# Optimization experiments

Hardware: AMD Instinct MI355X
Metric: run time of the kernel (lower is better)

## Reference

```python
import jax, jax.numpy as jnp
import numpy as np

B, H, W, C = 128, 28, 28, 512


def setup_inputs() -> dict:
    key = jax.random.key(0)
    k1, k2 = jax.random.split(key)
    x = jax.random.normal(k1, (B, H, W, C), dtype=jnp.float32)
    t_p = jax.random.uniform(k2, (H, W, H, W), dtype=jnp.float32)
    return {"x": x, "t_p": t_p}


def reference(x, t_p):
    # x: [B,H,W,C] NHWC; t_p: [H,W,H,W] spatial template bank.
    Bx, Hx, Wx, Cx = x.shape
    # Global-spatial max_pool_with_argmax == argmax over flattened H*W per (b,c).
    flat = x.reshape(Bx, Hx * Wx, Cx)
    idx = jnp.argmax(flat, axis=1)            # [B,C] first-max, like TF
    h = idx // Wx                              # [B,C] row of spatial argmax
    w = idx % Wx                               # [B,C] col of spatial argmax
    # Per-(b,c) template gather: t_p[h,w] -> [B,C,H,W]
    templates = t_p[h, w]
    templates = jnp.transpose(templates, (0, 2, 3, 1))  # [B,H,W,C]
    masked = jax.nn.relu(x * templates)
    return masked, x, templates
```

## Files before the change

### kernel.cpp

```cpp
#include <hip/hip_runtime.h>

#define Bn 128
#define Hn 28
#define Wn 28
#define Cn 512
#define Pn (Hn * Wn)
#define NCH 8
#define CB (Bn / NCH)
#define SCH 28
#define PCH (Pn / SCH)
#define ARGB ((CB / 2) * SCH)
#define MSKB (CB * 14)
#define PPB 56
#define PPT 28

typedef float f4 __attribute__((ext_vector_type(4)));

__device__ __forceinline__ void nt_store4(float* p, float a, float b, float c, float d) {
    f4 v = {a, b, c, d};
    __builtin_nontemporal_store(v, reinterpret_cast<f4*>(p));
}
__device__ __forceinline__ f4 nt_load4(const float* p) {
    return __builtin_nontemporal_load(reinterpret_cast<const f4*>(p));
}

__global__ __launch_bounds__(256) void pipe(const float* __restrict__ x,
                                            const float* __restrict__ tp,
                                            float* __restrict__ o0,
                                            float* __restrict__ o1,
                                            float* __restrict__ o2,
                                            uint2* __restrict__ part,
                                            int k, int nArg) {
    __shared__ int sidx[Cn];

    if ((int)blockIdx.x < nArg) {
        int blk = blockIdx.x;
        int s  = blk % SCH;
        int bp = blk / SCH;
        int bl = bp * 2 + (threadIdx.x >> 7);
        int b  = k * CB + bl;
        int c0 = (threadIdx.x & 127) * 4;

        size_t base = (size_t)b * Pn * Cn + c0;
        int p0 = s * PCH;

        float b0 = -INFINITY, b1 = -INFINITY, b2 = -INFINITY, b3 = -INFINITY;
        int i0 = p0, i1 = p0, i2 = p0, i3 = p0;
#pragma unroll 7
        for (int i = 0; i < PCH; ++i) {
            float4 v = *reinterpret_cast<const float4*>(x + base + (size_t)(p0 + i) * Cn);
            if (v.x > b0) { b0 = v.x; i0 = p0 + i; }
            if (v.y > b1) { b1 = v.y; i1 = p0 + i; }
            if (v.z > b2) { b2 = v.z; i2 = p0 + i; }
            if (v.w > b3) { b3 = v.w; i3 = p0 + i; }
        }
        uint2* o = part + (((size_t)(k & 1) * SCH + s) * CB + bl) * Cn + c0;
        o[0] = make_uint2(__float_as_uint(b0), (unsigned)i0);
        o[1] = make_uint2(__float_as_uint(b1), (unsigned)i1);
        o[2] = make_uint2(__float_as_uint(b2), (unsigned)i2);
        o[3] = make_uint2(__float_as_uint(b3), (unsigned)i3);
        return;
    }

    int blk = blockIdx.x - nArg;
    int pc = blk % 14;
    int bl = blk / 14;
    int b  = (k - 1) * CB + bl;
    int t  = threadIdx.x;

    if (t < 128) {
        int c0 = t * 4;
        const uint2* pp = part + ((size_t)((k - 1) & 1) * SCH * CB + bl) * Cn + c0;
        float v0 = -INFINITY, v1 = -INFINITY, v2 = -INFINITY, v3 = -INFINITY;
        int j0 = 0, j1 = 0, j2 = 0, j3 = 0;
#pragma unroll
        for (int s = 0; s < SCH; ++s) {
            const uint2* q = pp + (size_t)s * (CB * Cn);
            uint4 a = *reinterpret_cast<const uint4*>(q);
            uint4 c = *reinterpret_cast<const uint4*>(q + 2);
            float f0 = __uint_as_float(a.x), f1 = __uint_as_float(a.z);
            float f2 = __uint_as_float(c.x), f3 = __uint_as_float(c.z);
            if (f0 > v0) { v0 = f0; j0 = (int)a.y; }
            if (f1 > v1) { v1 = f1; j1 = (int)a.w; }
            if (f2 > v2) { v2 = f2; j2 = (int)c.y; }
            if (f3 > v3) { v3 = f3; j3 = (int)c.w; }
        }
        sidx[c0 + 0] = j0;
        sidx[c0 + 1] = j1;
        sidx[c0 + 2] = j2;
        sidx[c0 + 3] = j3;
    }
    __syncthreads();

    int ci = t & 127;
    int c0 = ci * 4;
    int ph = t >> 7;
    int p0 = pc * PPB + ph * PPT;

    int4 iv = *reinterpret_cast<const int4*>(sidx + c0);
    const float* t0p = tp + (size_t)iv.x * Pn;
    const float* t1p = tp + (size_t)iv.y * Pn;
    const float* t2p = tp + (size_t)iv.z * Pn;
    const float* t3p = tp + (size_t)iv.w * Pn;

    size_t xbase = (size_t)b * Pn * Cn + c0;

#pragma unroll
    for (int j = 0; j < PPT; j += 4) {
        int p = p0 + j;
        float4 ta = *reinterpret_cast<const float4*>(t0p + p);
        float4 tb = *reinterpret_cast<const float4*>(t1p + p);
        float4 tc = *reinterpret_cast<const float4*>(t2p + p);
        float4 td = *reinterpret_cast<const float4*>(t3p + p);
        f4 x0 = nt_load4(x + xbase + (size_t)(p + 0) * Cn);
        f4 x1 = nt_load4(x + xbase + (size_t)(p + 1) * Cn);
        f4 x2 = nt_load4(x + xbase + (size_t)(p + 2) * Cn);
        f4 x3 = nt_load4(x + xbase + (size_t)(p + 3) * Cn);

        size_t q0 = xbase + (size_t)(p + 0) * Cn;
        size_t q1 = xbase + (size_t)(p + 1) * Cn;
        size_t q2 = xbase + (size_t)(p + 2) * Cn;
        size_t q3 = xbase + (size_t)(p + 3) * Cn;

        nt_store4(o1 + q0, x0.x, x0.y, x0.z, x0.w);
        nt_store4(o1 + q1, x1.x, x1.y, x1.z, x1.w);
        nt_store4(o1 + q2, x2.x, x2.y, x2.z, x2.w);
        nt_store4(o1 + q3, x3.x, x3.y, x3.z, x3.w);
        nt_store4(o0 + q0, fmaxf(x0.x * ta.x, 0.f), fmaxf(x0.y * tb.x, 0.f),
                           fmaxf(x0.z * tc.x, 0.f), fmaxf(x0.w * td.x, 0.f));
        nt_store4(o0 + q1, fmaxf(x1.x * ta.y, 0.f), fmaxf(x1.y * tb.y, 0.f),
                           fmaxf(x1.z * tc.y, 0.f), fmaxf(x1.w * td.y, 0.f));
        nt_store4(o0 + q2, fmaxf(x2.x * ta.z, 0.f), fmaxf(x2.y * tb.z, 0.f),
                           fmaxf(x2.z * tc.z, 0.f), fmaxf(x2.w * td.z, 0.f));
        nt_store4(o0 + q3, fmaxf(x3.x * ta.w, 0.f), fmaxf(x3.y * tb.w, 0.f),
                           fmaxf(x3.z * tc.w, 0.f), fmaxf(x3.w * td.w, 0.f));
        nt_store4(o2 + q0, ta.x, tb.x, tc.x, td.x);
        nt_store4(o2 + q1, ta.y, tb.y, tc.y, td.y);
        nt_store4(o2 + q2, ta.z, tb.z, tc.z, td.z);
        nt_store4(o2 + q3, ta.w, tb.w, tc.w, td.w);
    }
}

extern "C" void kernel_launch(void* const* d_in, const int* in_sizes, int n_in,
                              void* d_out, int out_size, void* d_ws, size_t ws_size,
                              hipStream_t stream) {
    const float* x  = (const float*)d_in[0];
    const float* tp = (const float*)d_in[1];

    const size_t N = (size_t)Bn * Pn * Cn;
    float* o0 = (float*)d_out;
    float* o1 = o0 + N;
    float* o2 = o0 + 2 * N;

    uint2* part = (uint2*)d_ws;

    for (int k = 0; k <= NCH; ++k) {
        int nArg  = (k < NCH) ? ARGB : 0;
        int nMask = (k > 0) ? MSKB : 0;
        pipe<<<nArg + nMask, 256, 0, stream>>>(x, tp, o0, o1, o2, part, k, nArg);
    }
}
```

Baseline: 195.7 us.

## Replace chunked pipelined launches with two separate argmax and mask kernels

Drops the 9-launch software pipeline that overlapped the argmax pass for one batch chunk with the mask/output pass for the previous chunk. It now runs one argmax-partial kernel over all batches with 8 spatial splits and 128-thread blocks, then a single mask kernel. This removes per-launch overhead and the mixed-role blocks. It gives up the cross-chunk overlap and the L2 reuse of x between the two passes, so x is likely read from HBM twice.

```diff
diff --git a/kernel.cpp b/kernel.cpp
--- a/kernel.cpp
+++ b/kernel.cpp
@@ -5,12 +5,8 @@
 #define Wn 28
 #define Cn 512
 #define Pn (Hn * Wn)
-#define NCH 8
-#define CB (Bn / NCH)
-#define SCH 28
+#define SCH 8
 #define PCH (Pn / SCH)
-#define ARGB ((CB / 2) * SCH)
-#define MSKB (CB * 14)
 #define PPB 56
 #define PPT 28
 
@@ -24,58 +20,52 @@
     return __builtin_nontemporal_load(reinterpret_cast<const f4*>(p));
 }
 
-__global__ __launch_bounds__(256) void pipe(const float* __restrict__ x,
-                                            const float* __restrict__ tp,
-                                            float* __restrict__ o0,
-                                            float* __restrict__ o1,
-                                            float* __restrict__ o2,
-                                            uint2* __restrict__ part,
-                                            int k, int nArg) {
+__global__ void argmax_partial(const float* __restrict__ x,
+                               uint2* __restrict__ part) {
+    int s = blockIdx.x & (SCH - 1);
+    int b = blockIdx.x >> 3;
+    int c0 = threadIdx.x * 4;
+
+    const float* xp = x + (size_t)b * Pn * Cn + c0;
+    int p0 = s * PCH;
+
+    float b0 = -INFINITY, b1 = -INFINITY, b2 = -INFINITY, b3 = -INFINITY;
+    int i0 = p0, i1 = p0, i2 = p0, i3 = p0;
+#pragma unroll 7
+    for (int i = 0; i < PCH; ++i) {
+        float4 v = *reinterpret_cast<const float4*>(xp + (size_t)(p0 + i) * Cn);
+        if (v.x > b0) { b0 = v.x; i0 = p0 + i; }
+        if (v.y > b1) { b1 = v.y; i1 = p0 + i; }
+        if (v.z > b2) { b2 = v.z; i2 = p0 + i; }
+        if (v.w > b3) { b3 = v.w; i3 = p0 + i; }
+    }
+    uint4* o = reinterpret_cast<uint4*>(part + ((size_t)s * Bn + b) * Cn + c0);
+    o[0] = make_uint4(__float_as_uint(b0), (unsigned)i0,
+                      __float_as_uint(b1), (unsigned)i1);
+    o[1] = make_uint4(__float_as_uint(b2), (unsigned)i2,
+                      __float_as_uint(b3), (unsigned)i3);
+}
+
+__global__ void mask_outputs(const float* __restrict__ x,
+                             const float* __restrict__ tp,
+                             const uint2* __restrict__ part,
+                             float* __restrict__ o0,
+                             float* __restrict__ o1,
+                             float* __restrict__ o2) {
     __shared__ int sidx[Cn];
 
-    if ((int)blockIdx.x < nArg) {
-        int blk = blockIdx.x;
-        int s  = blk % SCH;
-        int bp = blk / SCH;
-        int bl = bp * 2 + (threadIdx.x >> 7);
-        int b  = k * CB + bl;
-        int c0 = (threadIdx.x & 127) * 4;
-
-        size_t base = (size_t)b * Pn * Cn + c0;
-        int p0 = s * PCH;
-
-        float b0 = -INFINITY, b1 = -INFINITY, b2 = -INFINITY, b3 = -INFINITY;
-        int i0 = p0, i1 = p0, i2 = p0, i3 = p0;
-#pragma unroll 7
-        for (int i = 0; i < PCH; ++i) {
-            float4 v = *reinterpret_cast<const float4*>(x + base + (size_t)(p0 + i) * Cn);
-            if (v.x > b0) { b0 = v.x; i0 = p0 + i; }
-            if (v.y > b1) { b1 = v.y; i1 = p0 + i; }
-            if (v.z > b2) { b2 = v.z; i2 = p0 + i; }
-            if (v.w > b3) { b3 = v.w; i3 = p0 + i; }
-        }
-        uint2* o = part + (((size_t)(k & 1) * SCH + s) * CB + bl) * Cn + c0;
-        o[0] = make_uint2(__float_as_uint(b0), (unsigned)i0);
-        o[1] = make_uint2(__float_as_uint(b1), (unsigned)i1);
-        o[2] = make_uint2(__float_as_uint(b2), (unsigned)i2);
-        o[3] = make_uint2(__float_as_uint(b3), (unsigned)i3);
-        return;
-    }
-
-    int blk = blockIdx.x - nArg;
-    int pc = blk % 14;
-    int bl = blk / 14;
-    int b  = (k - 1) * CB + bl;
+    int pc = blockIdx.x % 14;
+    int b  = blockIdx.x / 14;
     int t  = threadIdx.x;
 
     if (t < 128) {
         int c0 = t * 4;
-        const uint2* pp = part + ((size_t)((k - 1) & 1) * SCH * CB + bl) * Cn + c0;
+        const uint2* pp = part + (size_t)b * Cn + c0;
         float v0 = -INFINITY, v1 = -INFINITY, v2 = -INFINITY, v3 = -INFINITY;
         int j0 = 0, j1 = 0, j2 = 0, j3 = 0;
 #pragma unroll
         for (int s = 0; s < SCH; ++s) {
-            const uint2* q = pp + (size_t)s * (CB * Cn);
+            const uint2* q = pp + (size_t)s * (Bn * Cn);
             uint4 a = *reinterpret_cast<const uint4*>(q);
             uint4 c = *reinterpret_cast<const uint4*>(q + 2);
             float f0 = __uint_as_float(a.x), f1 = __uint_as_float(a.z);
@@ -154,9 +144,6 @@
 
     uint2* part = (uint2*)d_ws;
 
-    for (int k = 0; k <= NCH; ++k) {
-        int nArg  = (k < NCH) ? ARGB : 0;
-        int nMask = (k > 0) ? MSKB : 0;
-        pipe<<<nArg + nMask, 256, 0, stream>>>(x, tp, o0, o1, o2, part, k, nArg);
-    }
+    argmax_partial<<<Bn * SCH, 128, 0, stream>>>(x, part);
+    mask_outputs<<<Bn * 14, 256, 0, stream>>>(x, tp, part, o0, o1, o2);
 }
```

Result: faster. 165.9 us (-15.2%).
